# Optimization experiments

Hardware: AMD Instinct MI355X
Metric: run time of the kernel (lower is better)

The kernel has to match this reference:

```python
import jax, jax.numpy as jnp
import numpy as np

B, T, U, NOUT = 64, 512, 256, 4


def lstm(x, W, Uh, b):
    """Keras-style LSTM. x: [B,T,F]. Returns (seq [B,T,U], last [B,U]).
    Gate order i, f, g(candidate), o; sigmoid recurrent activation, tanh activation."""
    xz = jnp.einsum('btf,fg->btg', x, W) + b  # precompute input projections [B,T,4U]

    def step(carry, xz_t):
        h, c = carry
        z = xz_t + h @ Uh
        i, f, g, o = jnp.split(z, 4, axis=-1)
        i = jax.nn.sigmoid(i)
        f = jax.nn.sigmoid(f)
        g = jnp.tanh(g)
        o = jax.nn.sigmoid(o)
        c = f * c + i * g
        h = o * jnp.tanh(c)
        return (h, c), h

    h0 = jnp.zeros((x.shape[0], Uh.shape[0]), x.dtype)
    (h_last, _), hs = jax.lax.scan(step, (h0, h0), jnp.swapaxes(xz, 0, 1))
    return jnp.swapaxes(hs, 0, 1), h_last


def setup_inputs() -> dict:
    key = jax.random.key(0)
    ks = jax.random.split(key, 7)
    s_in = 1.0 / np.sqrt(U)
    return {
        'x': jax.random.normal(ks[0], (B, T, U), jnp.float32),
        'Wr': jax.random.normal(ks[1], (U, 4 * U), jnp.float32) * s_in,
        'Ur': jax.random.normal(ks[2], (U, 4 * U), jnp.float32) * s_in,
        'br': jnp.zeros((4 * U,), jnp.float32),
        'Wn': jax.random.normal(ks[3], (U, 4 * U), jnp.float32) * s_in,
        'Un': jax.random.normal(ks[4], (U, 4 * U), jnp.float32) * s_in,
        'bn': jnp.zeros((4 * U,), jnp.float32),
        'Wd': jax.random.normal(ks[5], (T * U, NOUT), jnp.float32) * (1.0 / np.sqrt(T * U)),
        'bd': jnp.zeros((NOUT,), jnp.float32),
    }


def reference(x, Wr, Ur, br, Wn, Un, bn, Wd, bd):
    # n_hidden = 3, inference (training=False): noise/dropout are identity.
    # Layer 0: shared return-sequences LSTM, no residual.
    h0, _ = lstm(x, Wr, Ur, br)                      # [B,T,U]
    # Layer 1: SAME shared LSTM weights, residual add.
    h1, _ = lstm(h0, Wr, Ur, br)
    h1 = h1 + h0                                     # [B,T,U]
    # Layer 2 (last): non-returning LSTM; residual Add broadcasts [B,U] + [B,T,U].
    _, h2 = lstm(h1, Wn, Un, bn)                     # [B,U]
    y = h2[:, None, :] + h1                          # [B,T,U]
    y = y.reshape(y.shape[0], -1)                    # flatten -> [B, T*U]
    return y @ Wd + bd                               # [B, NOUT]
```

## Files before the change

### kernel.cpp

```cpp
#include <hip/hip_runtime.h>
#include <hip/hip_fp16.h>
#include <cstddef>
#include <cstdint>

#define U_DIM 256
#define G_DIM 1024
#define T_DIM 512
#define B_DIM 64
#define TC    64
#define NCHUNK (T_DIM / TC)
#define NSLOT  (NCHUNK + 2)
#define BHID   (B_DIM * U_DIM)
#define NPART  8

#define NG_TOT 32
#define NG_REG 23
#define NG_LDS 9

typedef _Float16 half2v __attribute__((ext_vector_type(2)));

__device__ __forceinline__ float fsig(float x) {
    return 1.0f / (1.0f + __expf(-x));
}
__device__ __forceinline__ float ftanh(float x) {
    return 2.0f * fsig(2.0f * x) - 1.0f;
}

#define PIN4(v) asm("" : "+v"(v.x), "+v"(v.y), "+v"(v.z), "+v"(v.w))

__global__ __launch_bounds__(256)
void pack_w(const float* __restrict__ U, uint4* __restrict__ P)
{
    const int idx = blockIdx.x * 256 + threadIdx.x;
    const int g = idx >> 10;
    const int n = idx & 1023;
    uint vals[4];
    #pragma unroll
    for (int j = 0; j < 4; ++j) {
        const int k = g * 8 + j * 2;
        const __half a = __float2half_rn(U[(size_t)k * G_DIM + n]);
        const __half b = __float2half_rn(U[(size_t)(k + 1) * G_DIM + n]);
        const unsigned short ua = __builtin_bit_cast(unsigned short, a);
        const unsigned short ub = __builtin_bit_cast(unsigned short, b);
        vals[j] = (uint)ua | ((uint)ub << 16);
    }
    P[idx] = make_uint4(vals[0], vals[1], vals[2], vals[3]);
}

__device__ __forceinline__ float mac8(float acc, uint4 w, uint4 h)
{
#if __has_builtin(__builtin_amdgcn_fdot2)
    acc = __builtin_amdgcn_fdot2(__builtin_bit_cast(half2v, h.x),
                                 __builtin_bit_cast(half2v, w.x), acc, false);
    acc = __builtin_amdgcn_fdot2(__builtin_bit_cast(half2v, h.y),
                                 __builtin_bit_cast(half2v, w.y), acc, false);
    acc = __builtin_amdgcn_fdot2(__builtin_bit_cast(half2v, h.z),
                                 __builtin_bit_cast(half2v, w.z), acc, false);
    acc = __builtin_amdgcn_fdot2(__builtin_bit_cast(half2v, h.w),
                                 __builtin_bit_cast(half2v, w.w), acc, false);
#else
    const uint wv[4] = {w.x, w.y, w.z, w.w};
    const uint hv[4] = {h.x, h.y, h.z, h.w};
    #pragma unroll
    for (int j = 0; j < 4; ++j) {
        const __half2 wp = __builtin_bit_cast(__half2, wv[j]);
        const __half2 hp = __builtin_bit_cast(__half2, hv[j]);
        acc += __half2float(hp.x) * __half2float(wp.x);
        acc += __half2float(hp.y) * __half2float(wp.y);
    }
#endif
    return acc;
}

__global__
__attribute__((amdgpu_flat_work_group_size(512, 512)))
__attribute__((amdgpu_waves_per_eu(2, 2)))
void lstm_pipe(int slot,
               const __half* __restrict__ xzAll,
               const uint4* __restrict__ Pr, const uint4* __restrict__ Pn,
               __half* __restrict__ h0, __half* __restrict__ h1,
               float* __restrict__ hsAll, float* __restrict__ csAll)
{
    const int layer = blockIdx.x >> 6;
    const int b     = blockIdx.x & 63;
    const int c     = slot - layer;
    if ((unsigned)c >= (unsigned)NCHUNK) return;
    const int t0 = c * TC;

    const uint4* __restrict__ P = (layer < 2) ? Pr : Pn;
    const __half* __restrict__ xzb =
        xzAll + (size_t)layer * (B_DIM * TC * G_DIM) + (size_t)b * TC * G_DIM;
    const __half* __restrict__ resb =
        (layer == 1) ? (h0 + (size_t)(b * T_DIM + t0) * U_DIM) : nullptr;
    __half* __restrict__ outb =
        (layer == 0) ? (h0 + (size_t)(b * T_DIM + t0) * U_DIM)
      : (layer == 1) ? (h1 + (size_t)(b * T_DIM + t0) * U_DIM) : nullptr;
    float* __restrict__ hstate = hsAll + (size_t)layer * BHID + b * U_DIM;
    float* __restrict__ cstate = csAll + (size_t)layer * BHID + b * U_DIM;

    const int t = threadIdx.x;
    const int n0 = t;
    const int n1 = t + 512;

    __shared__ __align__(16) uint hq[U_DIM / 2];
    __shared__ float csh[U_DIM];
    __shared__ float zsh[G_DIM];
    __shared__ uint4 wlds[NG_LDS][G_DIM];

    uint4 wA[NG_REG], wB[NG_REG];
    #pragma unroll
    for (int g = 0; g < NG_REG; ++g) {
        wA[g] = P[(size_t)g * G_DIM + n0];
        wB[g] = P[(size_t)g * G_DIM + n1];
    }
    #pragma unroll
    for (int g = 0; g < NG_REG; ++g) { PIN4(wA[g]); PIN4(wB[g]); }
    #pragma unroll
    for (int g = 0; g < NG_LDS; ++g) {
        wlds[g][n0] = P[(size_t)(NG_REG + g) * G_DIM + n0];
        wlds[g][n1] = P[(size_t)(NG_REG + g) * G_DIM + n1];
    }

    if (t < U_DIM) {
        float hv, cv;
        if (c == 0) { hv = 0.0f; cv = 0.0f; }
        else        { hv = hstate[t]; cv = cstate[t]; }
        csh[t] = cv;
        ((__half*)hq)[t] = __float2half_rn(hv);
    }
    __syncthreads();

    float cur0 = __half2float(xzb[n0]);
    float cur1 = __half2float(xzb[n1]);
    float resv = (resb && t < U_DIM) ? __half2float(resb[t]) : 0.0f;

    for (int tl = 0; tl < TC; ++tl) {
        float acc0 = cur0;
        float acc1 = cur1;

        const int tn = (tl + 1 < TC) ? (tl + 1) : (TC - 1);
        cur0 = __half2float(xzb[(size_t)tn * G_DIM + n0]);
        cur1 = __half2float(xzb[(size_t)tn * G_DIM + n1]);
        const float resn = (resb && t < U_DIM)
                         ? __half2float(resb[(size_t)tn * U_DIM + t]) : 0.0f;

        const uint4* __restrict__ hp = (const uint4*)hq;

        #pragma unroll
        for (int g = 0; g < NG_REG; ++g) {
            const uint4 h4 = hp[g];
            acc0 = mac8(acc0, wA[g], h4);
            acc1 = mac8(acc1, wB[g], h4);
        }
        #pragma unroll
        for (int g = 0; g < NG_LDS; ++g) {
            const uint4 h4 = hp[NG_REG + g];
            acc0 = mac8(acc0, wlds[g][n0], h4);
            acc1 = mac8(acc1, wlds[g][n1], h4);
        }

        zsh[n0] = fsig(acc0);
        zsh[n1] = (t < U_DIM) ? ftanh(acc1) : fsig(acc1);
        __syncthreads();

        if (t < U_DIM) {
            const float iv = zsh[t];
            const float fv = zsh[t + 256];
            const float gv = zsh[t + 512];
            const float ov = zsh[t + 768];
            const float cc = fv * csh[t] + iv * gv;
            const float hh = ov * ftanh(cc);
            csh[t] = cc;
            ((__half*)hq)[t] = __float2half_rn(hh);
            if (outb) outb[(size_t)tl * U_DIM + t] = __float2half_rn(hh + resv);
        }
        resv = resn;
        __syncthreads();
    }

    if (t < U_DIM) {
        hstate[t] = __half2float(((const __half*)hq)[t]);
        cstate[t] = csh[t];
    }
}

__global__ __launch_bounds__(256)
void gemm3(int slot,
           const float* __restrict__ x,
           const __half* __restrict__ h0, const __half* __restrict__ h1,
           const float* __restrict__ Wr, const float* __restrict__ Wn,
           const float* __restrict__ br, const float* __restrict__ bn,
           __half* __restrict__ xzAll)
{
    const int z = blockIdx.z;
    const int c = slot - z;
    if ((unsigned)c >= (unsigned)NCHUNK) return;
    const int t0 = c * TC;

    const float*  W    = (z < 2) ? Wr : Wn;
    const float*  bias = (z < 2) ? br : bn;
    const __half* Ah   = (z == 1) ? h0 : h1;
    __half* out = xzAll + (size_t)z * (B_DIM * TC * G_DIM);

    __shared__ float As[16][64];
    __shared__ float Bs[16][64];

    const int tid = threadIdx.x;
    const int bm = blockIdx.y * 64;
    const int bn_ = blockIdx.x * 64;

    const int arow = tid >> 2;
    const int acol = (tid & 3) << 2;
    const int m_local = bm + arow;
    const int b  = m_local >> 6;
    const int tl = m_local & (TC - 1);
    const size_t grow = (size_t)(b * T_DIM + t0 + tl) * U_DIM;

    const int brow = tid >> 4;
    const int bcol = (tid & 15) << 2;

    const int tr = tid >> 4;
    const int tc = tid & 15;

    float acc[4][4] = {};

    for (int k0 = 0; k0 < U_DIM; k0 += 16) {
        float av[4];
        if (z == 0) {
            const float4 a4 = *(const float4*)(x + grow + k0 + acol);
            av[0] = a4.x; av[1] = a4.y; av[2] = a4.z; av[3] = a4.w;
        } else {
            const ushort4 a4 = *(const ushort4*)(Ah + grow + k0 + acol);
            av[0] = __half2float(__builtin_bit_cast(__half, a4.x));
            av[1] = __half2float(__builtin_bit_cast(__half, a4.y));
            av[2] = __half2float(__builtin_bit_cast(__half, a4.z));
            av[3] = __half2float(__builtin_bit_cast(__half, a4.w));
        }
        const float4 b4 = *(const float4*)(W + (size_t)(k0 + brow) * G_DIM + bn_ + bcol);
        As[acol + 0][arow] = av[0];
        As[acol + 1][arow] = av[1];
        As[acol + 2][arow] = av[2];
        As[acol + 3][arow] = av[3];
        *(float4*)&Bs[brow][bcol] = b4;
        __syncthreads();
        #pragma unroll
        for (int k = 0; k < 16; ++k) {
            const float4 a2 = *(const float4*)&As[k][tr << 2];
            const float4 b2 = *(const float4*)&Bs[k][tc << 2];
            const float a_[4] = {a2.x, a2.y, a2.z, a2.w};
            const float b_[4] = {b2.x, b2.y, b2.z, b2.w};
            #pragma unroll
            for (int i = 0; i < 4; ++i)
                #pragma unroll
                for (int j = 0; j < 4; ++j)
                    acc[i][j] += a_[i] * b_[j];
        }
        __syncthreads();
    }

    const int oc = bn_ + (tc << 2);
    const float4 bia = *(const float4*)(bias + oc);
    #pragma unroll
    for (int i = 0; i < 4; ++i) {
        const int m = bm + (tr << 2) + i;
        ushort4 o;
        o.x = __builtin_bit_cast(unsigned short, __float2half_rn(acc[i][0] + bia.x));
        o.y = __builtin_bit_cast(unsigned short, __float2half_rn(acc[i][1] + bia.y));
        o.z = __builtin_bit_cast(unsigned short, __float2half_rn(acc[i][2] + bia.z));
        o.w = __builtin_bit_cast(unsigned short, __float2half_rn(acc[i][3] + bia.w));
        *(ushort4*)(out + (size_t)m * G_DIM + oc) = o;
    }
}

__global__ __launch_bounds__(256)
void final_partial(const __half* __restrict__ h1, const float* __restrict__ h2,
                   const float* __restrict__ Wd, float* __restrict__ partials)
{
    const int b = blockIdx.x;
    const int p = blockIdx.y;
    const int tid = threadIdx.x;
    const int JTOT = T_DIM * U_DIM;
    const int JPART = JTOT / NPART;

    const __half* hb = h1 + (size_t)b * JTOT;
    const float* h2b = h2 + (size_t)b * U_DIM;

    float a0 = 0.f, a1 = 0.f, a2 = 0.f, a3 = 0.f;

    for (int j = p * JPART + tid * 8; j < (p + 1) * JPART; j += 256 * 8) {
        const uint4 hv = *(const uint4*)(hb + j);
        const int m = j & (U_DIM - 1);
        const float4 s0 = *(const float4*)(h2b + m);
        const float4 s1 = *(const float4*)(h2b + m + 4);
        float v[8];
        {
            const __half2 p0 = __builtin_bit_cast(__half2, hv.x);
            const __half2 p1 = __builtin_bit_cast(__half2, hv.y);
            const __half2 p2 = __builtin_bit_cast(__half2, hv.z);
            const __half2 p3 = __builtin_bit_cast(__half2, hv.w);
            v[0] = __half2float(p0.x) + s0.x;
            v[1] = __half2float(p0.y) + s0.y;
            v[2] = __half2float(p1.x) + s0.z;
            v[3] = __half2float(p1.y) + s0.w;
            v[4] = __half2float(p2.x) + s1.x;
            v[5] = __half2float(p2.y) + s1.y;
            v[6] = __half2float(p3.x) + s1.z;
            v[7] = __half2float(p3.y) + s1.w;
        }
        #pragma unroll
        for (int u = 0; u < 8; ++u) {
            const float4 w = *(const float4*)&Wd[(size_t)(j + u) * 4];
            a0 += v[u] * w.x;
            a1 += v[u] * w.y;
            a2 += v[u] * w.z;
            a3 += v[u] * w.w;
        }
    }

    __shared__ float red[256][4];
    red[tid][0] = a0; red[tid][1] = a1; red[tid][2] = a2; red[tid][3] = a3;
    __syncthreads();
    for (int s = 128; s > 0; s >>= 1) {
        if (tid < s) {
            #pragma unroll
            for (int o = 0; o < 4; ++o) red[tid][o] += red[tid + s][o];
        }
        __syncthreads();
    }
    if (tid < 4) partials[((size_t)b * NPART + p) * 4 + tid] = red[0][tid];
}

__global__ __launch_bounds__(256)
void final_reduce(const float* __restrict__ partials, const float* __restrict__ bd,
                  float* __restrict__ y)
{
    const int tid = threadIdx.x;
    const int b = tid >> 2;
    const int o = tid & 3;
    float s = bd[o];
    #pragma unroll
    for (int p = 0; p < NPART; ++p)
        s += partials[((size_t)b * NPART + p) * 4 + o];
    y[b * 4 + o] = s;
}

extern "C" void kernel_launch(void* const* d_in, const int* in_sizes, int n_in,
                              void* d_out, int out_size, void* d_ws, size_t ws_size,
                              hipStream_t stream)
{
    (void)in_sizes; (void)n_in; (void)out_size; (void)ws_size;

    const float* x  = (const float*)d_in[0];
    const float* Wr = (const float*)d_in[1];
    const float* Ur = (const float*)d_in[2];
    const float* br = (const float*)d_in[3];
    const float* Wn = (const float*)d_in[4];
    const float* Un = (const float*)d_in[5];
    const float* bn = (const float*)d_in[6];
    const float* Wd = (const float*)d_in[7];
    const float* bd = (const float*)d_in[8];
    float* y = (float*)d_out;

    char* wp = (char*)d_ws;
    uint4* Pr = (uint4*)wp;                       wp += (size_t)NG_TOT * G_DIM * 16;
    uint4* Pn = (uint4*)wp;                       wp += (size_t)NG_TOT * G_DIM * 16;
    float* hsAll = (float*)wp;                    wp += (size_t)3 * BHID * 4;
    float* csAll = (float*)wp;                    wp += (size_t)3 * BHID * 4;
    float* partials = (float*)wp;                 wp += (size_t)B_DIM * NPART * 4 * 4;
    __half* xzAll = (__half*)wp;                  wp += (size_t)3 * B_DIM * TC * G_DIM * 2;
    __half* h0 = (__half*)wp;                     wp += (size_t)B_DIM * T_DIM * U_DIM * 2;
    __half* h1 = (__half*)wp;                     wp += (size_t)B_DIM * T_DIM * U_DIM * 2;

    pack_w<<<128, 256, 0, stream>>>(Ur, Pr);
    pack_w<<<128, 256, 0, stream>>>(Un, Pn);

    dim3 ggrid(G_DIM / 64, (B_DIM * TC) / 64, 3);
    for (int slot = 0; slot < NSLOT; ++slot) {
        gemm3<<<ggrid, 256, 0, stream>>>(slot, x, h0, h1, Wr, Wn, br, bn, xzAll);
        lstm_pipe<<<3 * B_DIM, 512, 0, stream>>>(slot, xzAll, Pr, Pn,
                                                 h0, h1, hsAll, csAll);
    }

    final_partial<<<dim3(B_DIM, NPART), 256, 0, stream>>>(h1, hsAll + 2 * BHID,
                                                          Wd, partials);
    final_reduce<<<1, 256, 0, stream>>>(partials, bd, y);
}
```

Measured before the change: 1.951 ms.

## Use fp16 MFMA for input-projection GEMM with packed weights and fp16 x

Replaces the fp32 LDS-tiled SIMT GEMM computing input projections with a matrix-core kernel using mfma_f32_16x16x32_f16. Fragments load directly from global memory. The input weights are pre-packed into fp16 pairs in the same layout as the recurrent weights, and x is converted to fp16 once up front. This targets the per-slot GEMM compute cost, which sits on the pipeline critical path alongside the recurrent kernel. It adds extra packing kernels and workspace, and lowers the precision of the x projection to fp16.

```diff
diff --git a/kernel.cpp b/kernel.cpp
--- a/kernel.cpp
+++ b/kernel.cpp
@@ -18,6 +18,8 @@
 #define NG_LDS 9
 
 typedef _Float16 half2v __attribute__((ext_vector_type(2)));
+typedef _Float16 f16x8  __attribute__((ext_vector_type(8)));
+typedef float    f32x4  __attribute__((ext_vector_type(4)));
 
 __device__ __forceinline__ float fsig(float x) {
     return 1.0f / (1.0f + __expf(-x));
@@ -45,6 +47,25 @@
         vals[j] = (uint)ua | ((uint)ub << 16);
     }
     P[idx] = make_uint4(vals[0], vals[1], vals[2], vals[3]);
+}
+
+__global__ __launch_bounds__(256)
+void pack_x(const float* __restrict__ x, __half* __restrict__ xh)
+{
+    const size_t i = ((size_t)blockIdx.x * 256 + threadIdx.x) * 8;
+    const float4 a = *(const float4*)(x + i);
+    const float4 b = *(const float4*)(x + i + 4);
+    ushort4 o0, o1;
+    o0.x = __builtin_bit_cast(unsigned short, __float2half_rn(a.x));
+    o0.y = __builtin_bit_cast(unsigned short, __float2half_rn(a.y));
+    o0.z = __builtin_bit_cast(unsigned short, __float2half_rn(a.z));
+    o0.w = __builtin_bit_cast(unsigned short, __float2half_rn(a.w));
+    o1.x = __builtin_bit_cast(unsigned short, __float2half_rn(b.x));
+    o1.y = __builtin_bit_cast(unsigned short, __float2half_rn(b.y));
+    o1.z = __builtin_bit_cast(unsigned short, __float2half_rn(b.z));
+    o1.w = __builtin_bit_cast(unsigned short, __float2half_rn(b.w));
+    *(ushort4*)(xh + i) = o0;
+    *(ushort4*)(xh + i + 4) = o1;
 }
 
 __device__ __forceinline__ float mac8(float acc, uint4 w, uint4 h)
@@ -185,90 +206,65 @@
 }
 
 __global__ __launch_bounds__(256)
-void gemm3(int slot,
-           const float* __restrict__ x,
-           const __half* __restrict__ h0, const __half* __restrict__ h1,
-           const float* __restrict__ Wr, const float* __restrict__ Wn,
-           const float* __restrict__ br, const float* __restrict__ bn,
-           __half* __restrict__ xzAll)
+void gemm3_mfma(int slot,
+                const __half* __restrict__ xh,
+                const __half* __restrict__ h0, const __half* __restrict__ h1,
+                const uint4* __restrict__ PWr, const uint4* __restrict__ PWn,
+                const float* __restrict__ br, const float* __restrict__ bn,
+                __half* __restrict__ xzAll)
 {
     const int z = blockIdx.z;
     const int c = slot - z;
     if ((unsigned)c >= (unsigned)NCHUNK) return;
     const int t0 = c * TC;
 
-    const float*  W    = (z < 2) ? Wr : Wn;
-    const float*  bias = (z < 2) ? br : bn;
-    const __half* Ah   = (z == 1) ? h0 : h1;
-    __half* out = xzAll + (size_t)z * (B_DIM * TC * G_DIM);
-
-    __shared__ float As[16][64];
-    __shared__ float Bs[16][64];
+    const __half* __restrict__ A = (z == 0) ? xh : ((z == 1) ? h0 : h1);
+    const uint4*  __restrict__ PW = (z < 2) ? PWr : PWn;
+    const float*  __restrict__ bias = (z < 2) ? br : bn;
+    __half* __restrict__ out = xzAll + (size_t)z * (B_DIM * TC * G_DIM);
 
     const int tid = threadIdx.x;
+    const int w = tid >> 6;
+    const int l = tid & 63;
+
     const int bm = blockIdx.y * 64;
     const int bn_ = blockIdx.x * 64;
-
-    const int arow = tid >> 2;
-    const int acol = (tid & 3) << 2;
-    const int m_local = bm + arow;
-    const int b  = m_local >> 6;
-    const int tl = m_local & (TC - 1);
-    const size_t grow = (size_t)(b * T_DIM + t0 + tl) * U_DIM;
-
-    const int brow = tid >> 4;
-    const int bcol = (tid & 15) << 2;
-
-    const int tr = tid >> 4;
-    const int tc = tid & 15;
-
-    float acc[4][4] = {};
-
-    for (int k0 = 0; k0 < U_DIM; k0 += 16) {
-        float av[4];
-        if (z == 0) {
-            const float4 a4 = *(const float4*)(x + grow + k0 + acol);
-            av[0] = a4.x; av[1] = a4.y; av[2] = a4.z; av[3] = a4.w;
-        } else {
-            const ushort4 a4 = *(const ushort4*)(Ah + grow + k0 + acol);
-            av[0] = __half2float(__builtin_bit_cast(__half, a4.x));
-            av[1] = __half2float(__builtin_bit_cast(__half, a4.y));
-            av[2] = __half2float(__builtin_bit_cast(__half, a4.z));
-            av[3] = __half2float(__builtin_bit_cast(__half, a4.w));
-        }
-        const float4 b4 = *(const float4*)(W + (size_t)(k0 + brow) * G_DIM + bn_ + bcol);
-        As[acol + 0][arow] = av[0];
-        As[acol + 1][arow] = av[1];
-        As[acol + 2][arow] = av[2];
-        As[acol + 3][arow] = av[3];
-        *(float4*)&Bs[brow][bcol] = b4;
-        __syncthreads();
-        #pragma unroll
-        for (int k = 0; k < 16; ++k) {
-            const float4 a2 = *(const float4*)&As[k][tr << 2];
-            const float4 b2 = *(const float4*)&Bs[k][tc << 2];
-            const float a_[4] = {a2.x, a2.y, a2.z, a2.w};
-            const float b_[4] = {b2.x, b2.y, b2.z, b2.w};
-            #pragma unroll
-            for (int i = 0; i < 4; ++i)
-                #pragma unroll
-                for (int j = 0; j < 4; ++j)
-                    acc[i][j] += a_[i] * b_[j];
-        }
-        __syncthreads();
-    }
-
-    const int oc = bn_ + (tc << 2);
-    const float4 bia = *(const float4*)(bias + oc);
-    #pragma unroll
-    for (int i = 0; i < 4; ++i) {
-        const int m = bm + (tr << 2) + i;
-        ushort4 o;
-        o.x = __builtin_bit_cast(unsigned short, __float2half_rn(acc[i][0] + bia.x));
-        o.y = __builtin_bit_cast(unsigned short, __float2half_rn(acc[i][1] + bia.y));
-        o.z = __builtin_bit_cast(unsigned short, __float2half_rn(acc[i][2] + bia.z));
-        o.w = __builtin_bit_cast(unsigned short, __float2half_rn(acc[i][3] + bia.w));
-        *(ushort4*)(out + (size_t)m * G_DIM + oc) = o;
+    const int col = bn_ + w * 16 + (l & 15);
+    const int krow = l >> 4;
+
+    const __half* arow[4];
+    #pragma unroll
+    for (int rt = 0; rt < 4; ++rt) {
+        const int m = bm + rt * 16 + (l & 15);
+        const int b = m >> 6;
+        const int tl = m & (TC - 1);
+        arow[rt] = A + (size_t)(b * T_DIM + t0 + tl) * U_DIM + krow * 8;
+    }
+
+    f32x4 acc[4] = {{0,0,0,0},{0,0,0,0},{0,0,0,0},{0,0,0,0}};
+
+    #pragma unroll
+    for (int kt = 0; kt < 8; ++kt) {
+        const uint4 bfrag = PW[(size_t)(4 * kt + krow) * G_DIM + col];
+        #pragma unroll
+        for (int rt = 0; rt < 4; ++rt) {
+            const uint4 afrag = *(const uint4*)(arow[rt] + kt * 32);
+            acc[rt] = __builtin_amdgcn_mfma_f32_16x16x32_f16(
+                __builtin_bit_cast(f16x8, afrag), __builtin_bit_cast(f16x8, bfrag),
+                acc[rt], 0, 0, 0);
+        }
+    }
+
+    const float bv = bias[col];
+    #pragma unroll
+    for (int rt = 0; rt < 4; ++rt) {
+        #pragma unroll
+        for (int r = 0; r < 4; ++r) {
+            const int m = bm + rt * 16 + 4 * (l >> 4) + r;
+            const int b = m >> 6;
+            const int tl = m & (TC - 1);
+            out[(size_t)(b * TC + tl) * G_DIM + col] = __float2half_rn(acc[rt][r] + bv);
+        }
     }
 }
 
@@ -309,11 +305,11 @@
         }
         #pragma unroll
         for (int u = 0; u < 8; ++u) {
-            const float4 w = *(const float4*)&Wd[(size_t)(j + u) * 4];
-            a0 += v[u] * w.x;
-            a1 += v[u] * w.y;
-            a2 += v[u] * w.z;
-            a3 += v[u] * w.w;
+            const float4 wv = *(const float4*)&Wd[(size_t)(j + u) * 4];
+            a0 += v[u] * wv.x;
+            a1 += v[u] * wv.y;
+            a2 += v[u] * wv.z;
+            a3 += v[u] * wv.w;
         }
     }
 
@@ -362,21 +358,28 @@
     float* y = (float*)d_out;
 
     char* wp = (char*)d_ws;
-    uint4* Pr = (uint4*)wp;                       wp += (size_t)NG_TOT * G_DIM * 16;
-    uint4* Pn = (uint4*)wp;                       wp += (size_t)NG_TOT * G_DIM * 16;
+    uint4* Pr  = (uint4*)wp;                      wp += (size_t)NG_TOT * G_DIM * 16;
+    uint4* Pn  = (uint4*)wp;                      wp += (size_t)NG_TOT * G_DIM * 16;
+    uint4* PWr = (uint4*)wp;                      wp += (size_t)NG_TOT * G_DIM * 16;
+    uint4* PWn = (uint4*)wp;                      wp += (size_t)NG_TOT * G_DIM * 16;
     float* hsAll = (float*)wp;                    wp += (size_t)3 * BHID * 4;
     float* csAll = (float*)wp;                    wp += (size_t)3 * BHID * 4;
     float* partials = (float*)wp;                 wp += (size_t)B_DIM * NPART * 4 * 4;
     __half* xzAll = (__half*)wp;                  wp += (size_t)3 * B_DIM * TC * G_DIM * 2;
     __half* h0 = (__half*)wp;                     wp += (size_t)B_DIM * T_DIM * U_DIM * 2;
     __half* h1 = (__half*)wp;                     wp += (size_t)B_DIM * T_DIM * U_DIM * 2;
+    __half* xh = (__half*)wp;                     wp += (size_t)B_DIM * T_DIM * U_DIM * 2;
 
     pack_w<<<128, 256, 0, stream>>>(Ur, Pr);
     pack_w<<<128, 256, 0, stream>>>(Un, Pn);
+    pack_w<<<128, 256, 0, stream>>>(Wr, PWr);
+    pack_w<<<128, 256, 0, stream>>>(Wn, PWn);
+    pack_x<<<(B_DIM * T_DIM * U_DIM) / (256 * 8), 256, 0, stream>>>(x, xh);
 
     dim3 ggrid(G_DIM / 64, (B_DIM * TC) / 64, 3);
     for (int slot = 0; slot < NSLOT; ++slot) {
-        gemm3<<<ggrid, 256, 0, stream>>>(slot, x, h0, h1, Wr, Wn, br, bn, xzAll);
+        gemm3_mfma<<<ggrid, 256, 0, stream>>>(slot, xh, h0, h1, PWr, PWn,
+                                              br, bn, xzAll);
         lstm_pipe<<<3 * B_DIM, 512, 0, stream>>>(slot, xzAll, Pr, Pn,
                                                  h0, h1, hsAll, csAll);
     }
```

New measurement: 1.700 ms. -12.9%, faster.
